# Kernel optimization log

Measured on AMD Instinct MI355X. Metric: run time of the kernel, lower is better.

## Reference

```python
import jax, jax.numpy as jnp
import numpy as np

D_MODEL = 64
NUM_MODES = 16
SCALE = 1.0 / (D_MODEL * D_MODEL)


def setup_inputs() -> dict:
    key = jax.random.key(0)
    kq, kk, kv = jax.random.split(key, 3)
    shape = (4, 2048, 64, 64)  # (b, t, c, mw_dim)
    q = jax.random.normal(kq, shape, dtype=jnp.float32)
    k = jax.random.normal(kk, shape, dtype=jnp.float32)
    v = jax.random.normal(kv, shape, dtype=jnp.float32)
    return {"q": q, "k": k, "v": v}


def reference(q, k, v):
    b, t, c, mw = q.shape
    modes = min(t // 2, NUM_MODES)
    # permute (b,t,c,mw) -> (b,h,d,t) with h=mw_dim, d=c
    xq = jnp.transpose(q, (0, 3, 2, 1))
    xk = jnp.transpose(k, (0, 3, 2, 1))
    xv = jnp.transpose(v, (0, 3, 2, 1))
    # rfft over time, keep lowest `modes` frequency bins (contiguous low-pass)
    qf = jnp.fft.rfft(xq, axis=-1)[..., :modes]  # (b,h,d,modes) complex64
    kf = jnp.fft.rfft(xk, axis=-1)[..., :modes]
    vf = jnp.fft.rfft(xv, axis=-1)[..., :modes]
    # complex-domain attention over the reduced mode set
    qk = jnp.einsum('bhdx,bhdy->bhxy', qf, kf)  # (b,h,modes,modes)
    qk = jnp.tanh(qk)  # complex tanh, matching torch.tanh on cfloat
    qkv = jnp.einsum('bhxy,bhdy->bhdx', qk, vf)  # (b,h,d,modes)
    # scatter back into full rfft spectrum (zeros elsewhere)
    out_ft = jnp.zeros((b, mw, c, t // 2 + 1), dtype=qkv.dtype)
    out_ft = out_ft.at[..., :modes].set(qkv)
    out = jnp.fft.irfft(out_ft * SCALE, n=t, axis=-1)  # (b,h,d,t) float32
    return jnp.transpose(out, (0, 3, 2, 1))  # (b,t,c,mw)
```

## Files before the change

### kernel.cpp

```cpp
#include <hip/hip_runtime.h>
#include <hip/hip_bf16.h>
#include <math.h>


#define T_DIM 2048
#define DH 4096
#define DH2 2048
#define CH 8
#define TPCH 64
#define NT 4
#define NPH (TPCH / NT)
#define TT 16

__device__ inline float4 f4add(float4 a, float4 b) {
    return make_float4(a.x + b.x, a.y + b.y, a.z + b.z, a.w + b.w);
}
__device__ inline float4 f4sub(float4 a, float4 b) {
    return make_float4(a.x - b.x, a.y - b.y, a.z - b.z, a.w - b.w);
}

__global__ void init_tables(float* __restrict__ WA, float* __restrict__ Bt2) {
    int i = blockIdx.x * 256 + threadIdx.x;
    const float TWO_PI = 6.2831853071795864769f;
    if (i < 512 * 32) {
        int t = i >> 5, r = i & 31, m = r >> 1;
        int ph = (m * t) & 2047;
        float ang = TWO_PI * (float)ph * (1.0f / 2048.0f);
        WA[i] = (r & 1) ? sinf(ang) : cosf(ang);
    }
    int i2 = i - 512 * 32;
    if (i2 >= 0 && i2 < 1024 * 32) {
        int t = i2 >> 5, r = i2 & 31, m = r >> 1;
        int ph = (m * t) & 2047;
        float ang = TWO_PI * (float)ph * (1.0f / 2048.0f);
        const float S2 = 1.0f / (4096.0f * 2048.0f);
        float coef = (m == 0 ? 1.0f : 2.0f) * S2;
        float val;
        if (!(r & 1)) val = coef * cosf(ang);
        else          val = (m == 0) ? 0.0f : -coef * sinf(ang);
        Bt2[i2] = val;
    }
}

__global__ __launch_bounds__(256) void stageA(
        const float* __restrict__ q, const float* __restrict__ k,
        const float* __restrict__ v, const float* __restrict__ WA,
        float* __restrict__ P) {
    __shared__ float elds[2][NT][4][256];

    int tid  = threadIdx.x;
    int bx   = blockIdx.x;
    int c    = blockIdx.y;
    int tz   = blockIdx.z;
    int tensor = tz >> 2, b = tz & 3;
    int iw   = tid >> 6;
    int lane = tid & 63;

    const float* srcf = (tensor == 0 ? q : tensor == 1 ? k : v)
                        + (size_t)b * T_DIM * DH;
    const float4* src4 = (const float4*)srcf;
    int f4base = bx * 64 + lane;

    float accR[16], accI[16];
    #pragma unroll
    for (int m = 0; m < 16; m++) { accR[m] = 0.f; accI[m] = 0.f; }

    {
        int t0 = c * TPCH + iw;
        float4 x0 = src4[(size_t)t0 * 1024 + f4base];
        float4 x1 = src4[(size_t)(t0 + 512) * 1024 + f4base];
        float4 x2 = src4[(size_t)(t0 + 1024) * 1024 + f4base];
        float4 x3 = src4[(size_t)(t0 + 1536) * 1024 + f4base];
        float4 u0 = f4add(x0, x2), u1 = f4add(x1, x3);
        float4 dd0 = f4sub(x0, x2), dd1 = f4sub(x1, x3);
        ((float4*)&elds[0][iw][0][0])[lane] = f4add(u0, u1);
        ((float4*)&elds[0][iw][1][0])[lane] = f4sub(u0, u1);
        ((float4*)&elds[0][iw][2][0])[lane] = dd0;
        ((float4*)&elds[0][iw][3][0])[lane] = dd1;
    }
    __syncthreads();

    for (int ph = 0; ph < NPH; ph++) {
        float4 n0, n1, n2, n3;
        const bool has_next = (ph < NPH - 1);
        if (has_next) {
            int t0 = c * TPCH + (ph + 1) * NT + iw;
            n0 = src4[(size_t)t0 * 1024 + f4base];
            n1 = src4[(size_t)(t0 + 512) * 1024 + f4base];
            n2 = src4[(size_t)(t0 + 1024) * 1024 + f4base];
            n3 = src4[(size_t)(t0 + 1536) * 1024 + f4base];
        }
        int bsel = ph & 1;
        #pragma unroll
        for (int i = 0; i < NT; i++) {
            float ee  = elds[bsel][i][0][tid];
            float ff  = elds[bsel][i][1][tid];
            float dd0 = elds[bsel][i][2][tid];
            float dd1 = elds[bsel][i][3][tid];
            const float* tw = WA + (size_t)(c * TPCH + ph * NT + i) * 32;
            #pragma unroll
            for (int m = 0; m < 16; m++) {
                float cm = tw[2 * m], sm = tw[2 * m + 1];
                if ((m & 3) == 0) {
                    accR[m] = fmaf(cm, ee, accR[m]);
                    accI[m] = fmaf(-sm, ee, accI[m]);
                } else if ((m & 3) == 2) {
                    accR[m] = fmaf(cm, ff, accR[m]);
                    accI[m] = fmaf(-sm, ff, accI[m]);
                } else if ((m & 3) == 1) {
                    accR[m] = fmaf(cm, dd0, fmaf(-sm, dd1, accR[m]));
                    accI[m] = fmaf(-sm, dd0, fmaf(-cm, dd1, accI[m]));
                } else {
                    accR[m] = fmaf(cm, dd0, fmaf(sm, dd1, accR[m]));
                    accI[m] = fmaf(-sm, dd0, fmaf(cm, dd1, accI[m]));
                }
            }
        }
        if (has_next) {
            int nb = (ph + 1) & 1;
            float4 u0 = f4add(n0, n2), u1 = f4add(n1, n3);
            float4 dd0 = f4sub(n0, n2), dd1 = f4sub(n1, n3);
            ((float4*)&elds[nb][iw][0][0])[lane] = f4add(u0, u1);
            ((float4*)&elds[nb][iw][1][0])[lane] = f4sub(u0, u1);
            ((float4*)&elds[nb][iw][2][0])[lane] = dd0;
            ((float4*)&elds[nb][iw][3][0])[lane] = dd1;
            __syncthreads();
        }
    }

    float* pp = P + ((size_t)(tz * CH + c) * 32) * DH + bx * 256 + tid;
    #pragma unroll
    for (int m = 0; m < 16; m++) {
        pp[(size_t)m * DH]        = accR[m];
        pp[(size_t)(16 + m) * DH] = accI[m];
    }
}

__global__ __launch_bounds__(256) void reduceP(const float4* __restrict__ P,
                                               float4* __restrict__ Y) {
    size_t i   = (size_t)blockIdx.x * 256 + threadIdx.x;
    size_t tzj = i >> 10;
    size_t dh4 = i & 1023;
    size_t tz  = tzj >> 5;
    size_t j   = tzj & 31;
    const float4* p = P + ((tz * CH) * 32 + j) * 1024 + dh4;
    float4 s = make_float4(0.f, 0.f, 0.f, 0.f);
    #pragma unroll
    for (int cc = 0; cc < CH; cc++) {
        float4 t = p[(size_t)cc * 32 * 1024];
        s.x += t.x; s.y += t.y; s.z += t.z; s.w += t.w;
    }
    Y[i] = s;
}

__global__ __launch_bounds__(256) void stageB(const float* __restrict__ Y,
                                              float* __restrict__ G) {
    __shared__ float qf[64 * 33];
    __shared__ float kf[64 * 33];
    __shared__ float vf[64 * 33];
    __shared__ float qkr[16 * 17];
    __shared__ float qki[16 * 17];

    int tid = threadIdx.x;
    int bh  = blockIdx.x;
    int b   = bh >> 6;
    int h   = bh & 63;

    #pragma unroll
    for (int tensor = 0; tensor < 3; tensor++) {
        float* dst = (tensor == 0 ? qf : tensor == 1 ? kf : vf);
        const float* yp = Y + ((size_t)(tensor * 4 + b) * 32) * DH + h;
        #pragma unroll
        for (int it = 0; it < 8; it++) {
            int p = it * 256 + tid;
            int d = p & 63, j = p >> 6;
            dst[d * 33 + j] = yp[(size_t)j * DH + d * 64];
        }
    }
    __syncthreads();

    int x = tid >> 4, y = tid & 15;
    float ar = 0.f, ai = 0.f;
    #pragma unroll 4
    for (int d = 0; d < 64; d++) {
        float qr = qf[d * 33 + x],      qi = qf[d * 33 + 16 + x];
        float kr = kf[d * 33 + y],      ki = kf[d * 33 + 16 + y];
        ar += qr * kr - qi * ki;
        ai += qr * ki + qi * kr;
    }
    float re, im;
    float a2 = 2.f * ar, b2 = 2.f * ai;
    if (fabsf(a2) < 80.f) {
        float den = coshf(a2) + cosf(b2);
        re = sinhf(a2) / den;
        im = sinf(b2) / den;
    } else {
        re = copysignf(1.f, ar);
        im = 0.f;
    }
    qkr[x * 17 + y] = re;
    qki[x * 17 + y] = im;
    __syncthreads();

    int xx = tid & 15, db = tid >> 4;
    #pragma unroll
    for (int i = 0; i < 4; i++) {
        int d = db + i * 16;
        float cr = 0.f, ci = 0.f;
        #pragma unroll
        for (int yy = 0; yy < 16; yy++) {
            float tr = qkr[xx * 17 + yy], ti = qki[xx * 17 + yy];
            float vr = vf[d * 33 + yy],   vi = vf[d * 33 + 16 + yy];
            cr += tr * vr - ti * vi;
            ci += tr * vi + ti * vr;
        }
        G[((size_t)b * 32 + xx) * DH + d * 64 + h]      = cr;
        G[((size_t)b * 32 + 16 + xx) * DH + d * 64 + h] = ci;
    }
}

__global__ __launch_bounds__(256) void stageC(const float* __restrict__ G,
                                              const float* __restrict__ Bt2,
                                              float* __restrict__ out) {
    __shared__ float w[TT * 32];
    int tid = threadIdx.x;
    int c   = blockIdx.y;
    int b   = blockIdx.z;

    #pragma unroll
    for (int it = 0; it < TT * 32 / 256; it++)
        w[it * 256 + tid] = Bt2[c * (TT * 32) + it * 256 + tid];
    __syncthreads();

    int dh2 = blockIdx.x * 256 + tid;
    float2 gr[16], gi[16];
    const float2* gp = (const float2*)G + (size_t)b * 32 * DH2 + dh2;
    #pragma unroll
    for (int m = 0; m < 16; m++) {
        gr[m] = gp[(size_t)m * DH2];
        gi[m] = gp[(size_t)(16 + m) * DH2];
    }

    float2* o0 = (float2*)out + ((size_t)b * T_DIM + (size_t)c * TT) * DH2 + dh2;
    #pragma unroll 2
    for (int tl = 0; tl < TT; tl++) {
        const float* ww = &w[tl * 32];
        float2 E = make_float2(0.f, 0.f), O = make_float2(0.f, 0.f);
        #pragma unroll
        for (int m = 0; m < 16; m += 2) {
            E.x = fmaf(ww[2 * m],     gr[m].x, E.x);
            E.x = fmaf(ww[2 * m + 1], gi[m].x, E.x);
            E.y = fmaf(ww[2 * m],     gr[m].y, E.y);
            E.y = fmaf(ww[2 * m + 1], gi[m].y, E.y);
        }
        #pragma unroll
        for (int m = 1; m < 16; m += 2) {
            O.x = fmaf(ww[2 * m],     gr[m].x, O.x);
            O.x = fmaf(ww[2 * m + 1], gi[m].x, O.x);
            O.y = fmaf(ww[2 * m],     gr[m].y, O.y);
            O.y = fmaf(ww[2 * m + 1], gi[m].y, O.y);
        }
        o0[(size_t)tl * DH2] = make_float2(E.x + O.x, E.y + O.y);
        o0[(size_t)(tl + 1024) * DH2] = make_float2(E.x - O.x, E.y - O.y);
    }
}

extern "C" void kernel_launch(void* const* d_in, const int* in_sizes, int n_in,
                              void* d_out, int out_size, void* d_ws, size_t ws_size,
                              hipStream_t stream) {
    const float* q = (const float*)d_in[0];
    const float* k = (const float*)d_in[1];
    const float* v = (const float*)d_in[2];
    float* out = (float*)d_out;

    char* ws = (char*)d_ws;
    float* WA  = (float*)ws;
    float* Bt2 = (float*)(ws + 65536);
    const size_t base = 65536 + 131072;

    const size_t psz = (size_t)12 * CH * 32 * DH * 4;
    const size_t ysz = 6291456;
    float* P = (float*)(ws + base);
    float* Y = (float*)(ws + base + psz);
    float* G = (float*)(ws + base + psz + ysz);

    init_tables<<<192, 256, 0, stream>>>(WA, Bt2);
    stageA<<<dim3(16, CH, 12), 256, 0, stream>>>(q, k, v, WA, P);
    reduceP<<<1536, 256, 0, stream>>>((const float4*)P, (float4*)Y);
    stageB<<<256, 256, 0, stream>>>(Y, G);
    stageC<<<dim3(8, 64, 4), 256, 0, stream>>>(G, Bt2, out);
}
```

Before: 435.4 us.

## Make stageA LDS staging wave-private and double-prefetch without block barriers

The stageA Fourier-projection kernel now gives each wavefront its own LDS slab holding 4 time rows by 16 float4 columns. A wave only reads data it folded itself, so the block-wide __syncthreads between phases can go. Loads are software-pipelined two phases ahead with two register sets (a/b) and two LDS buffers per wave. The aim is to remove barrier stalls and hide global-load latency better. The cost is more live registers and narrower contiguous loads per row (256 B instead of 1 KB).

After: 481.1 us. 10.5% more time.

```diff
diff --git a/kernel.cpp b/kernel.cpp
--- a/kernel.cpp
+++ b/kernel.cpp
@@ -8,8 +8,7 @@
 #define DH2 2048
 #define CH 8
 #define TPCH 64
-#define NT 4
-#define NPH (TPCH / NT)
+#define NPH 16
 #define TT 16
 
 __device__ inline float4 f4add(float4 a, float4 b) {
@@ -42,91 +41,98 @@
     }
 }
 
+
+#define LOADP(PH, X0, X1, X2, X3) do {                                         \
+    size_t t0 = (size_t)(tbase + (PH) * 4);                                    \
+    X0 = src4[t0 * 1024 + f4];                                                 \
+    X1 = src4[(t0 + 512) * 1024 + f4];                                         \
+    X2 = src4[(t0 + 1024) * 1024 + f4];                                        \
+    X3 = src4[(t0 + 1536) * 1024 + f4];                                        \
+} while (0)
+
+#define FOLDW(BUF, X0, X1, X2, X3) do {                                        \
+    float4 fu0 = f4add(X0, X2), fu1 = f4add(X1, X3);                           \
+    float4 fd0 = f4sub(X0, X2), fd1 = f4sub(X1, X3);                           \
+    wslab[(BUF) * 256 + 0 * 64 + widx] = f4add(fu0, fu1);                      \
+    wslab[(BUF) * 256 + 1 * 64 + widx] = f4sub(fu0, fu1);                      \
+    wslab[(BUF) * 256 + 2 * 64 + widx] = fd0;                                  \
+    wslab[(BUF) * 256 + 3 * 64 + widx] = fd1;                                  \
+} while (0)
+
+#define COMP(BUF, PH) do {                                                     \
+    _Pragma("unroll")                                                          \
+    for (int i = 0; i < 4; i++) {                                              \
+        float ee  = elds[iw][BUF][0][i][lane];                                 \
+        float ff  = elds[iw][BUF][1][i][lane];                                 \
+        float dd0 = elds[iw][BUF][2][i][lane];                                 \
+        float dd1 = elds[iw][BUF][3][i][lane];                                 \
+        const float* tw = WA + (size_t)(c * TPCH + (PH) * 4 + i) * 32;         \
+        _Pragma("unroll")                                                      \
+        for (int m = 0; m < 16; m++) {                                         \
+            float cm = tw[2 * m], sm = tw[2 * m + 1];                          \
+            if ((m & 3) == 0) {                                                \
+                accR[m] = fmaf(cm, ee, accR[m]);                               \
+                accI[m] = fmaf(-sm, ee, accI[m]);                              \
+            } else if ((m & 3) == 2) {                                         \
+                accR[m] = fmaf(cm, ff, accR[m]);                               \
+                accI[m] = fmaf(-sm, ff, accI[m]);                              \
+            } else if ((m & 3) == 1) {                                         \
+                accR[m] = fmaf(cm, dd0, fmaf(-sm, dd1, accR[m]));              \
+                accI[m] = fmaf(-sm, dd0, fmaf(-cm, dd1, accI[m]));             \
+            } else {                                                           \
+                accR[m] = fmaf(cm, dd0, fmaf(sm, dd1, accR[m]));               \
+                accI[m] = fmaf(-sm, dd0, fmaf(cm, dd1, accI[m]));              \
+            }                                                                  \
+        }                                                                      \
+    }                                                                          \
+} while (0)
+
 __global__ __launch_bounds__(256) void stageA(
         const float* __restrict__ q, const float* __restrict__ k,
         const float* __restrict__ v, const float* __restrict__ WA,
         float* __restrict__ P) {
-    __shared__ float elds[2][NT][4][256];
+    __shared__ float elds[4][2][4][4][64];
 
     int tid  = threadIdx.x;
+    int iw   = tid >> 6;
+    int lane = tid & 63;
+    int li   = lane >> 4;
+    int lc   = lane & 15;
     int bx   = blockIdx.x;
     int c    = blockIdx.y;
     int tz   = blockIdx.z;
     int tensor = tz >> 2, b = tz & 3;
-    int iw   = tid >> 6;
-    int lane = tid & 63;
 
     const float* srcf = (tensor == 0 ? q : tensor == 1 ? k : v)
                         + (size_t)b * T_DIM * DH;
     const float4* src4 = (const float4*)srcf;
-    int f4base = bx * 64 + lane;
+    const int f4    = bx * 64 + iw * 16 + lc;
+    const int tbase = c * TPCH + li;
+
+    float4* wslab = (float4*)&elds[iw][0][0][0][0];
+    const int widx = li * 16 + lc;
 
     float accR[16], accI[16];
     #pragma unroll
     for (int m = 0; m < 16; m++) { accR[m] = 0.f; accI[m] = 0.f; }
 
-    {
-        int t0 = c * TPCH + iw;
-        float4 x0 = src4[(size_t)t0 * 1024 + f4base];
-        float4 x1 = src4[(size_t)(t0 + 512) * 1024 + f4base];
-        float4 x2 = src4[(size_t)(t0 + 1024) * 1024 + f4base];
-        float4 x3 = src4[(size_t)(t0 + 1536) * 1024 + f4base];
-        float4 u0 = f4add(x0, x2), u1 = f4add(x1, x3);
-        float4 dd0 = f4sub(x0, x2), dd1 = f4sub(x1, x3);
-        ((float4*)&elds[0][iw][0][0])[lane] = f4add(u0, u1);
-        ((float4*)&elds[0][iw][1][0])[lane] = f4sub(u0, u1);
-        ((float4*)&elds[0][iw][2][0])[lane] = dd0;
-        ((float4*)&elds[0][iw][3][0])[lane] = dd1;
-    }
-    __syncthreads();
-
-    for (int ph = 0; ph < NPH; ph++) {
-        float4 n0, n1, n2, n3;
-        const bool has_next = (ph < NPH - 1);
-        if (has_next) {
-            int t0 = c * TPCH + (ph + 1) * NT + iw;
-            n0 = src4[(size_t)t0 * 1024 + f4base];
-            n1 = src4[(size_t)(t0 + 512) * 1024 + f4base];
-            n2 = src4[(size_t)(t0 + 1024) * 1024 + f4base];
-            n3 = src4[(size_t)(t0 + 1536) * 1024 + f4base];
-        }
-        int bsel = ph & 1;
-        #pragma unroll
-        for (int i = 0; i < NT; i++) {
-            float ee  = elds[bsel][i][0][tid];
-            float ff  = elds[bsel][i][1][tid];
-            float dd0 = elds[bsel][i][2][tid];
-            float dd1 = elds[bsel][i][3][tid];
-            const float* tw = WA + (size_t)(c * TPCH + ph * NT + i) * 32;
-            #pragma unroll
-            for (int m = 0; m < 16; m++) {
-                float cm = tw[2 * m], sm = tw[2 * m + 1];
-                if ((m & 3) == 0) {
-                    accR[m] = fmaf(cm, ee, accR[m]);
-                    accI[m] = fmaf(-sm, ee, accI[m]);
-                } else if ((m & 3) == 2) {
-                    accR[m] = fmaf(cm, ff, accR[m]);
-                    accI[m] = fmaf(-sm, ff, accI[m]);
-                } else if ((m & 3) == 1) {
-                    accR[m] = fmaf(cm, dd0, fmaf(-sm, dd1, accR[m]));
-                    accI[m] = fmaf(-sm, dd0, fmaf(-cm, dd1, accI[m]));
-                } else {
-                    accR[m] = fmaf(cm, dd0, fmaf(sm, dd1, accR[m]));
-                    accI[m] = fmaf(-sm, dd0, fmaf(cm, dd1, accI[m]));
-                }
-            }
-        }
-        if (has_next) {
-            int nb = (ph + 1) & 1;
-            float4 u0 = f4add(n0, n2), u1 = f4add(n1, n3);
-            float4 dd0 = f4sub(n0, n2), dd1 = f4sub(n1, n3);
-            ((float4*)&elds[nb][iw][0][0])[lane] = f4add(u0, u1);
-            ((float4*)&elds[nb][iw][1][0])[lane] = f4sub(u0, u1);
-            ((float4*)&elds[nb][iw][2][0])[lane] = dd0;
-            ((float4*)&elds[nb][iw][3][0])[lane] = dd1;
-            __syncthreads();
-        }
-    }
+    float4 a0, a1, a2, a3, b0, b1, b2, b3;
+
+    LOADP(0, a0, a1, a2, a3);
+    FOLDW(0, a0, a1, a2, a3);
+    LOADP(1, b0, b1, b2, b3);
+
+    for (int ph = 0; ph < NPH - 2; ph += 2) {
+        LOADP(ph + 2, a0, a1, a2, a3);
+        COMP(0, ph);
+        FOLDW(1, b0, b1, b2, b3);
+        LOADP(ph + 3, b0, b1, b2, b3);
+        COMP(1, ph + 1);
+        FOLDW(0, a0, a1, a2, a3);
+    }
+    COMP(0, NPH - 2);
+    FOLDW(1, b0, b1, b2, b3);
+    COMP(1, NPH - 1);
 
     float* pp = P + ((size_t)(tz * CH + c) * 32) * DH + bx * 256 + tid;
     #pragma unroll
```
